# Optimization experiments

Measured on AMD Instinct MI355X. Metric: run time of the kernel, lower is better.

The kernel has to match this reference:

```python
import jax, jax.numpy as jnp
import numpy as np

B, H, S, D = 2, 16, 2048, 128

def setup_inputs() -> dict:
    key = jax.random.key(0)
    kq, kk, kv = jax.random.split(key, 3)
    q = jax.random.normal(kq, (B, H, S, D), dtype=jnp.float32)
    k = jax.random.normal(kk, (B, H, S, D), dtype=jnp.float32)
    v = jax.random.normal(kv, (B, H, S, D), dtype=jnp.float32)
    return {"q": q, "k": k, "v": v}

def reference(q, k, v):
    # scaled dot-product attention: softmax(q k^T / sqrt(d)) v
    scale = 1.0 / jnp.sqrt(jnp.asarray(q.shape[-1], q.dtype))
    scores = jnp.einsum('bhqd,bhkd->bhqk', q, k) * scale  # [B,H,S,S]
    probs = jax.nn.softmax(scores, axis=-1)
    attention = jnp.einsum('bhqk,bhkd->bhqd', probs, v)   # [B,H,S,D]
    return attention
```

## Files before the change

### kernel.cpp

```cpp
#include <hip/hip_runtime.h>

#define S_LEN 2048
#define D_DIM 128
#define NBH   32
#define KVB   64
#define QW    32
#define NW    8
#define QB    (QW*NW)
#define NQT   (S_LEN/QB)
#define NT    (S_LEN/KVB)

typedef __attribute__((ext_vector_type(8)))  short short8;
typedef __attribute__((ext_vector_type(16))) float f32x16;

__device__ __forceinline__ unsigned cvtpk(float a, float b) {
  unsigned r;
  asm("v_cvt_pk_bf16_f32 %0, %1, %2" : "=v"(r) : "v"(a), "v"(b));
  return r;
}
__device__ __forceinline__ float exp2fast(float x) {
#if __has_builtin(__builtin_amdgcn_exp2f)
  return __builtin_amdgcn_exp2f(x);
#else
  return exp2f(x);
#endif
}

__global__ __launch_bounds__(512, 2)
void attn_fwd(const float* __restrict__ Qf, const float* __restrict__ Kf,
              const float* __restrict__ Vf, float* __restrict__ Og) {
  __shared__ __attribute__((aligned(16))) unsigned short Ks[2 * KVB * D_DIM];
  __shared__ __attribute__((aligned(16))) unsigned short Vt[2 * D_DIM * KVB];

  const int tid  = threadIdx.x;
  const int lane = tid & 63;
  const int wid  = tid >> 6;
  const int l31  = lane & 31;
  const int hw   = lane >> 5;

  const int bid = blockIdx.x;
  const int bh  = (bid & 7) * 4 + ((bid >> 3) >> 3);
  const int qt  = (bid >> 3) & 7;
  const size_t base = (size_t)bh * (S_LEN * D_DIM);
  const int qrow = qt * QB + wid * QW + l31;

  short8 qb[8];
  {
    const float CS = 0.08838834764831845f * 1.44269504088896340f;
    const float* qp = Qf + base + (size_t)qrow * D_DIM + hw * 8;
#pragma unroll
    for (int c = 0; c < 8; ++c) {
      float4 x0 = *(const float4*)(qp + c * 16);
      float4 x1 = *(const float4*)(qp + c * 16 + 4);
      union { unsigned u[4]; short8 v; } w;
      w.u[0] = cvtpk(x0.x * CS, x0.y * CS); w.u[1] = cvtpk(x0.z * CS, x0.w * CS);
      w.u[2] = cvtpk(x1.x * CS, x1.y * CS); w.u[3] = cvtpk(x1.z * CS, x1.w * CS);
      qb[c] = w.v;
    }
  }

  f32x16 acc[4];
#pragma unroll
  for (int f = 0; f < 4; ++f)
#pragma unroll
    for (int r = 0; r < 16; ++r) acc[f][r] = 0.f;
  f32x16 lacc;
#pragma unroll
  for (int r = 0; r < 16; ++r) lacc[r] = 0.f;

  const int kr = tid >> 3;
  const int kc = (tid & 7) << 4;
  const int vr = (tid & 15) << 2;
  const int vc = (tid >> 4) << 2;

  float4 Kq0, Kq1, Kq2, Kq3;
  float4 Vq0, Vq1, Vq2, Vq3;

  const float* kpf = Kf + base + (size_t)kr * D_DIM + kc;
  const float* vpf = Vf + base + (size_t)vr * D_DIM + vc;

  auto LOAD = [&]() {
    Kq0 = *(const float4*)kpf;        Kq1 = *(const float4*)(kpf + 4);
    Kq2 = *(const float4*)(kpf + 8);  Kq3 = *(const float4*)(kpf + 12);
    Vq0 = *(const float4*)vpf;
    Vq1 = *(const float4*)(vpf + D_DIM);
    Vq2 = *(const float4*)(vpf + 2 * D_DIM);
    Vq3 = *(const float4*)(vpf + 3 * D_DIM);
    kpf += (size_t)KVB * D_DIM; vpf += (size_t)KVB * D_DIM;
  };

  auto STORE = [&](int p) {
    uint4 k0, k1;
    unsigned Vw0, Vw1, Vw2, Vw3, Vw4, Vw5, Vw6, Vw7;
    k0.x = cvtpk(Kq0.x, Kq0.y); k0.y = cvtpk(Kq0.z, Kq0.w);
    k0.z = cvtpk(Kq1.x, Kq1.y); k0.w = cvtpk(Kq1.z, Kq1.w);
    k1.x = cvtpk(Kq2.x, Kq2.y); k1.y = cvtpk(Kq2.z, Kq2.w);
    k1.z = cvtpk(Kq3.x, Kq3.y); k1.w = cvtpk(Kq3.z, Kq3.w);
    Vw0 = cvtpk(Vq0.x, Vq1.x); Vw1 = cvtpk(Vq2.x, Vq3.x);
    Vw2 = cvtpk(Vq0.y, Vq1.y); Vw3 = cvtpk(Vq2.y, Vq3.y);
    Vw4 = cvtpk(Vq0.z, Vq1.z); Vw5 = cvtpk(Vq2.z, Vq3.z);
    Vw6 = cvtpk(Vq0.w, Vq1.w); Vw7 = cvtpk(Vq2.w, Vq3.w);
    char* kdst = (char*)(Ks + p * (KVB * D_DIM));
    const int b0 = kr * 256 + kc * 2;
    const int sw = (kr & 7) << 4;
    *(uint4*)(kdst + (b0 ^ sw)) = k0;
    *(uint4*)(kdst + ((b0 + 16) ^ sw)) = k1;
    char* vdst = (char*)(Vt + p * (D_DIM * KVB));
    {
      const int d = vc;
      uint2 u; u.x = Vw0; u.y = Vw1;
      *(uint2*)(vdst + ((d * 128 + vr * 2) ^ ((d & 7) << 4))) = u;
    }
    {
      const int d = vc + 1;
      uint2 u; u.x = Vw2; u.y = Vw3;
      *(uint2*)(vdst + ((d * 128 + vr * 2) ^ ((d & 7) << 4))) = u;
    }
    {
      const int d = vc + 2;
      uint2 u; u.x = Vw4; u.y = Vw5;
      *(uint2*)(vdst + ((d * 128 + vr * 2) ^ ((d & 7) << 4))) = u;
    }
    {
      const int d = vc + 3;
      uint2 u; u.x = Vw6; u.y = Vw7;
      *(uint2*)(vdst + ((d * 128 + vr * 2) ^ ((d & 7) << 4))) = u;
    }
  };

  LOAD(); STORE(0); __syncthreads();
  int p = 0;
  for (int t = 0; t < NT; ++t) {
    if (t + 1 < NT) LOAD();

    const char* ksp = (const char*)(Ks + p * (KVB * D_DIM));
    const char* vtp = (const char*)(Vt + p * (D_DIM * KVB));
    const int asw = (l31 & 7) << 4;

    f32x16 s0, s1;
#pragma unroll
    for (int r = 0; r < 16; ++r) { s0[r] = 0.f; s1[r] = 0.f; }
    __builtin_amdgcn_s_setprio(1);
#pragma unroll
    for (int c = 0; c < 8; ++c) {
      const int byte = (l31 * 256 + c * 32 + hw * 16) ^ asw;
      short8 ka0 = *(const short8*)(ksp + byte);
      short8 ka1 = *(const short8*)(ksp + byte + 8192);
      s0 = __builtin_amdgcn_mfma_f32_32x32x16_bf16(ka0, qb[c], s0, 0, 0, 0);
      s1 = __builtin_amdgcn_mfma_f32_32x32x16_bf16(ka1, qb[c], s1, 0, 0, 0);
    }
    __builtin_amdgcn_s_setprio(0);

#pragma unroll
    for (int r = 0; r < 16; ++r) {
      s0[r] = exp2fast(s0[r]);
      s1[r] = exp2fast(s1[r]);
      lacc[r] += s0[r] + s1[r];
    }

#pragma unroll
    for (int t2 = 0; t2 < 4; ++t2) {
      unsigned w0, w1, w2, w3;
      if (t2 < 2) {
        const int rb = 8 * t2;
        w0 = cvtpk(s0[rb+0], s0[rb+1]); w1 = cvtpk(s0[rb+2], s0[rb+3]);
        w2 = cvtpk(s0[rb+4], s0[rb+5]); w3 = cvtpk(s0[rb+6], s0[rb+7]);
      } else {
        const int rb = 8 * (t2 - 2);
        w0 = cvtpk(s1[rb+0], s1[rb+1]); w1 = cvtpk(s1[rb+2], s1[rb+3]);
        w2 = cvtpk(s1[rb+4], s1[rb+5]); w3 = cvtpk(s1[rb+6], s1[rb+7]);
      }
      asm("v_permlane32_swap_b32 %0, %1" : "+v"(w0), "+v"(w2));
      asm("v_permlane32_swap_b32 %0, %1" : "+v"(w1), "+v"(w3));
      union { unsigned u[4]; short8 v; } pb;
      pb.u[0] = w0; pb.u[1] = w1; pb.u[2] = w2; pb.u[3] = w3;
      __builtin_amdgcn_s_setprio(1);
#pragma unroll
      for (int f = 0; f < 4; ++f) {
        const int byte = ((32 * f + l31) * 128 + t2 * 32 + hw * 16) ^ asw;
        short8 va = *(const short8*)(vtp + byte);
        acc[f] = __builtin_amdgcn_mfma_f32_32x32x16_bf16(va, pb.v, acc[f], 0, 0, 0);
      }
      __builtin_amdgcn_s_setprio(0);
    }

    if (t + 1 < NT) STORE(p ^ 1);
    __syncthreads();
    p ^= 1;
  }

  float tl[16];
#pragma unroll
  for (int r = 0; r < 16; ++r) tl[r] = lacc[r];
#pragma unroll
  for (int st = 8; st > 0; st >>= 1)
#pragma unroll
    for (int r = 0; r < st; ++r) tl[r] += tl[r + st];
  const float l = tl[0] + __shfl_xor(tl[0], 32);
  const float inv = 1.0f / l;
  float* op = Og + base + (size_t)qrow * D_DIM;
#pragma unroll
  for (int f = 0; f < 4; ++f)
#pragma unroll
    for (int g = 0; g < 4; ++g) {
      float4 o;
      o.x = acc[f][4*g+0] * inv; o.y = acc[f][4*g+1] * inv;
      o.z = acc[f][4*g+2] * inv; o.w = acc[f][4*g+3] * inv;
      *(float4*)(op + 32 * f + 8 * g + 4 * hw) = o;
    }
}

extern "C" void kernel_launch(void* const* d_in, const int* in_sizes, int n_in,
                              void* d_out, int out_size, void* d_ws, size_t ws_size,
                              hipStream_t stream) {
  const float* q = (const float*)d_in[0];
  const float* k = (const float*)d_in[1];
  const float* v = (const float*)d_in[2];
  float* out = (float*)d_out;
  attn_fwd<<<NBH * NQT, 512, 0, stream>>>(q, k, v, out);
}
```

Baseline: 85.15 us.

## Preconvert K to bf16 in workspace and load K fragments directly to registers

Adds a pre-pass kernel that converts K to bf16 in the workspace. The attention kernel then drops the K shared-memory tile and loads each wave's K MFMA operands straight from global memory into registers. This removes the LDS staging, its conversion work and LDS traffic for K, and halves K global bytes. In exchange it adds a separate kernel launch and a full K read/write pass. Every wave now re-reads K from global/L2 without cross-wave sharing, and register pressure rises from holding 16 K fragments.

```diff
diff --git a/kernel.cpp b/kernel.cpp
--- a/kernel.cpp
+++ b/kernel.cpp
@@ -26,10 +26,23 @@
 #endif
 }
 
+__global__ __launch_bounds__(256)
+void cvt_bf16(const float* __restrict__ src, unsigned* __restrict__ dst) {
+  const size_t i = (size_t)blockIdx.x * 256 + threadIdx.x;
+  const float4* s = (const float4*)src + i * 2;
+  float4 x0 = s[0], x1 = s[1];
+  uint4 u;
+  u.x = cvtpk(x0.x, x0.y); u.y = cvtpk(x0.z, x0.w);
+  u.z = cvtpk(x1.x, x1.y); u.w = cvtpk(x1.z, x1.w);
+  ((uint4*)dst)[i] = u;
+}
+
+template<bool PRE>
 __global__ __launch_bounds__(512, 2)
 void attn_fwd(const float* __restrict__ Qf, const float* __restrict__ Kf,
-              const float* __restrict__ Vf, float* __restrict__ Og) {
-  __shared__ __attribute__((aligned(16))) unsigned short Ks[2 * KVB * D_DIM];
+              const float* __restrict__ Vf,
+              const unsigned short* __restrict__ Kb,
+              float* __restrict__ Og) {
   __shared__ __attribute__((aligned(16))) unsigned short Vt[2 * D_DIM * KVB];
 
   const int tid  = threadIdx.x;
@@ -68,43 +81,26 @@
 #pragma unroll
   for (int r = 0; r < 16; ++r) lacc[r] = 0.f;
 
-  const int kr = tid >> 3;
-  const int kc = (tid & 7) << 4;
   const int vr = (tid & 15) << 2;
   const int vc = (tid >> 4) << 2;
 
-  float4 Kq0, Kq1, Kq2, Kq3;
   float4 Vq0, Vq1, Vq2, Vq3;
-
-  const float* kpf = Kf + base + (size_t)kr * D_DIM + kc;
   const float* vpf = Vf + base + (size_t)vr * D_DIM + vc;
 
-  auto LOAD = [&]() {
-    Kq0 = *(const float4*)kpf;        Kq1 = *(const float4*)(kpf + 4);
-    Kq2 = *(const float4*)(kpf + 8);  Kq3 = *(const float4*)(kpf + 12);
+  auto LOADV = [&]() {
     Vq0 = *(const float4*)vpf;
     Vq1 = *(const float4*)(vpf + D_DIM);
     Vq2 = *(const float4*)(vpf + 2 * D_DIM);
     Vq3 = *(const float4*)(vpf + 3 * D_DIM);
-    kpf += (size_t)KVB * D_DIM; vpf += (size_t)KVB * D_DIM;
+    vpf += (size_t)KVB * D_DIM;
   };
 
-  auto STORE = [&](int p) {
-    uint4 k0, k1;
+  auto STOREV = [&](int p) {
     unsigned Vw0, Vw1, Vw2, Vw3, Vw4, Vw5, Vw6, Vw7;
-    k0.x = cvtpk(Kq0.x, Kq0.y); k0.y = cvtpk(Kq0.z, Kq0.w);
-    k0.z = cvtpk(Kq1.x, Kq1.y); k0.w = cvtpk(Kq1.z, Kq1.w);
-    k1.x = cvtpk(Kq2.x, Kq2.y); k1.y = cvtpk(Kq2.z, Kq2.w);
-    k1.z = cvtpk(Kq3.x, Kq3.y); k1.w = cvtpk(Kq3.z, Kq3.w);
     Vw0 = cvtpk(Vq0.x, Vq1.x); Vw1 = cvtpk(Vq2.x, Vq3.x);
     Vw2 = cvtpk(Vq0.y, Vq1.y); Vw3 = cvtpk(Vq2.y, Vq3.y);
     Vw4 = cvtpk(Vq0.z, Vq1.z); Vw5 = cvtpk(Vq2.z, Vq3.z);
     Vw6 = cvtpk(Vq0.w, Vq1.w); Vw7 = cvtpk(Vq2.w, Vq3.w);
-    char* kdst = (char*)(Ks + p * (KVB * D_DIM));
-    const int b0 = kr * 256 + kc * 2;
-    const int sw = (kr & 7) << 4;
-    *(uint4*)(kdst + (b0 ^ sw)) = k0;
-    *(uint4*)(kdst + ((b0 + 16) ^ sw)) = k1;
     char* vdst = (char*)(Vt + p * (D_DIM * KVB));
     {
       const int d = vc;
@@ -128,12 +124,38 @@
     }
   };
 
-  LOAD(); STORE(0); __syncthreads();
+  const unsigned short* kbp = PRE ? (Kb + base + (size_t)l31 * D_DIM + hw * 8)
+                                  : nullptr;
+  const float*          kfp = PRE ? nullptr
+                                  : (Kf + base + (size_t)l31 * D_DIM + hw * 8);
+
+  LOADV(); STOREV(0); __syncthreads();
   int p = 0;
   for (int t = 0; t < NT; ++t) {
-    if (t + 1 < NT) LOAD();
-
-    const char* ksp = (const char*)(Ks + p * (KVB * D_DIM));
+    short8 ka0[8], ka1[8];
+    if constexpr (PRE) {
+#pragma unroll
+      for (int c = 0; c < 8; ++c) {
+        ka0[c] = *(const short8*)(kbp + c * 16);
+        ka1[c] = *(const short8*)(kbp + 32 * D_DIM + c * 16);
+      }
+    } else {
+#pragma unroll
+      for (int c = 0; c < 8; ++c) {
+        float4 a0 = *(const float4*)(kfp + c * 16);
+        float4 a1 = *(const float4*)(kfp + c * 16 + 4);
+        float4 b0 = *(const float4*)(kfp + 32 * D_DIM + c * 16);
+        float4 b1 = *(const float4*)(kfp + 32 * D_DIM + c * 16 + 4);
+        union { unsigned u[4]; short8 v; } wa, wb;
+        wa.u[0] = cvtpk(a0.x, a0.y); wa.u[1] = cvtpk(a0.z, a0.w);
+        wa.u[2] = cvtpk(a1.x, a1.y); wa.u[3] = cvtpk(a1.z, a1.w);
+        wb.u[0] = cvtpk(b0.x, b0.y); wb.u[1] = cvtpk(b0.z, b0.w);
+        wb.u[2] = cvtpk(b1.x, b1.y); wb.u[3] = cvtpk(b1.z, b1.w);
+        ka0[c] = wa.v; ka1[c] = wb.v;
+      }
+    }
+    if (t + 1 < NT) LOADV();
+
     const char* vtp = (const char*)(Vt + p * (D_DIM * KVB));
     const int asw = (l31 & 7) << 4;
 
@@ -143,11 +165,8 @@
     __builtin_amdgcn_s_setprio(1);
 #pragma unroll
     for (int c = 0; c < 8; ++c) {
-      const int byte = (l31 * 256 + c * 32 + hw * 16) ^ asw;
-      short8 ka0 = *(const short8*)(ksp + byte);
-      short8 ka1 = *(const short8*)(ksp + byte + 8192);
-      s0 = __builtin_amdgcn_mfma_f32_32x32x16_bf16(ka0, qb[c], s0, 0, 0, 0);
-      s1 = __builtin_amdgcn_mfma_f32_32x32x16_bf16(ka1, qb[c], s1, 0, 0, 0);
+      s0 = __builtin_amdgcn_mfma_f32_32x32x16_bf16(ka0[c], qb[c], s0, 0, 0, 0);
+      s1 = __builtin_amdgcn_mfma_f32_32x32x16_bf16(ka1[c], qb[c], s1, 0, 0, 0);
     }
     __builtin_amdgcn_s_setprio(0);
 
@@ -184,7 +203,10 @@
       __builtin_amdgcn_s_setprio(0);
     }
 
-    if (t + 1 < NT) STORE(p ^ 1);
+    if constexpr (PRE) kbp += (size_t)KVB * D_DIM;
+    else               kfp += (size_t)KVB * D_DIM;
+
+    if (t + 1 < NT) STOREV(p ^ 1);
     __syncthreads();
     p ^= 1;
   }
@@ -217,5 +239,13 @@
   const float* k = (const float*)d_in[1];
   const float* v = (const float*)d_in[2];
   float* out = (float*)d_out;
-  attn_fwd<<<NBH * NQT, 512, 0, stream>>>(q, k, v, out);
-}
+  const size_t nel  = (size_t)NBH * S_LEN * D_DIM;
+  const size_t need = nel * sizeof(unsigned short);
+  if (ws_size >= need) {
+    unsigned short* kb = (unsigned short*)d_ws;
+    cvt_bf16<<<(int)(nel / 8 / 256), 256, 0, stream>>>(k, (unsigned*)kb);
+    attn_fwd<true><<<NBH * NQT, 512, 0, stream>>>(q, k, v, kb, out);
+  } else {
+    attn_fwd<false><<<NBH * NQT, 512, 0, stream>>>(q, k, v, nullptr, out);
+  }
+}
```

New measurement: 190.4 us. 124% more time.
